# Kernel tuning notes

Hardware: AMD Instinct MI355X
Metric: run time of the kernel (lower is better)

The kernel has to match this reference:

```python
import jax, jax.numpy as jnp
import numpy as np

IN_DIM = 64
OUT_DIM = 64
N_MODES = 32


def setup_inputs() -> dict:
    key = jax.random.key(0)
    k_x, k_w0, k_w1 = jax.random.split(key, 3)
    x = jax.random.normal(k_x, (32, IN_DIM, 128, 128), dtype=jnp.float32)
    # xavier_normal_ on tensor of shape (in, out, modes, 2): fan_in = out*modes*2, fan_out = in*modes*2? 
    # torch treats dim0 as fan_out-ish; exact init scale is irrelevant for correctness baselines,
    # so use a matching gaussian std = sqrt(2/(in_dim+out_dim)).
    std = float(np.sqrt(2.0 / (IN_DIM + OUT_DIM)))
    w0 = std * jax.random.normal(k_w0, (IN_DIM, OUT_DIM, N_MODES, 2), dtype=jnp.float32)
    w1 = std * jax.random.normal(k_w1, (IN_DIM, OUT_DIM, N_MODES, 2), dtype=jnp.float32)
    return {"x": x, "w0": w0, "w1": w1}


def reference(x, w0, w1):
    B, I, M, N = x.shape
    n_modes = w0.shape[2]

    # ---- width (last-axis) branch ----
    x_fty = jnp.fft.rfft(x, axis=-1, norm='ortho')                      # [B, I, M, N//2+1]
    wc0 = w0[..., 0] + 1j * w0[..., 1]                                  # [I, O, n_modes]
    low_y = jnp.einsum('bixy,ioy->boxy', x_fty[..., :n_modes], wc0)     # [B, O, M, n_modes]
    out_ft_y = jnp.pad(low_y, ((0, 0), (0, 0), (0, 0), (0, N // 2 + 1 - n_modes)))
    xy = jnp.fft.irfft(out_ft_y, n=N, axis=-1, norm='ortho')            # [B, O, M, N]

    # ---- height (second-to-last axis) branch ----
    x_ftx = jnp.fft.rfft(x, axis=-2, norm='ortho')                      # [B, I, M//2+1, N]
    wc1 = w1[..., 0] + 1j * w1[..., 1]                                  # [I, O, n_modes]
    low_x = jnp.einsum('bixy,iox->boxy', x_ftx[:, :, :n_modes, :], wc1)  # [B, O, n_modes, N]
    out_ft_x = jnp.pad(low_x, ((0, 0), (0, 0), (0, M // 2 + 1 - n_modes), (0, 0)))
    xx = jnp.fft.irfft(out_ft_x, n=M, axis=-2, norm='ortho')            # [B, O, M, N]

    return xx + xy
```

## Files before the change

kernel.cpp:

```cpp
#include <hip/hip_runtime.h>


typedef _Float16 half8  __attribute__((ext_vector_type(8)));
typedef _Float16 half4v __attribute__((ext_vector_type(4)));
typedef _Float16 half2v __attribute__((ext_vector_type(2)));
typedef float    floatx4 __attribute__((ext_vector_type(4)));

#define TWO_PI_OVER_128 0.049087385212340517f

__device__ __forceinline__ unsigned int packh2(float a, float b) {
    half2v h; h[0] = (_Float16)a; h[1] = (_Float16)b;
    return __builtin_bit_cast(unsigned int, h);
}
__device__ __forceinline__ half8  ash8(uint4 u) { return __builtin_bit_cast(half8, u); }
__device__ __forceinline__ half4v ash4(uint2 u) { return __builtin_bit_cast(half4v, u); }

#define MFMA_K16(A,B,C) __builtin_amdgcn_mfma_f32_16x16x16f16((A),(B),(C),0,0,0)

#define YS_PK 324
#define YS_PR 20

__global__ __launch_bounds__(256) void w2expand(const float* __restrict__ w0,
                                                const float* __restrict__ w1,
                                                uint2* __restrict__ W2h)
{
    int g = blockIdx.x * 256 + threadIdx.x;
    const float* w = (g >> 17) ? w1 : w0;
    int e    = g & 131071;
    int lane = e & 63;
    int m    = (e >> 6) & 7;
    int c    = (e >> 9) & 7;
    int k    = e >> 12;
    int mrow = lane & 15, q = lane >> 4;
    int o  = (m * 16 + mrow) >> 1;
    int oc = mrow & 1;
    unsigned int h2[2];
#pragma unroll
    for (int hp = 0; hp < 2; ++hp) {
        int i = c * 8 + q * 2 + hp;
        const float* wp = w + ((i * 64 + o) * 32 + k) * 2;
        float re = wp[0], im = wp[1];
        float v0 = oc ? im : re;
        float v1 = oc ? re : -im;
        h2[hp] = packh2(v0, v1);
    }
    W2h[g] = make_uint2(h2[0], h2[1]);
}

template<int BR>
__global__ __launch_bounds__(1024, 4) void spectral(const float* __restrict__ x,
                                                    const uint2* __restrict__ w2,
                                                    float* __restrict__ out)
{
    __shared__ uint4 Ubuf[36864 / 16];
    __shared__ unsigned short Ys[32 * YS_PK];

    unsigned short* Xs = (unsigned short*)Ubuf;
    unsigned int*   Zs = (unsigned int*)Ubuf;

    const int tid  = threadIdx.x;
    const int wv   = tid >> 6;
    const int lane = tid & 63;
    const int mrow = tid & 15;
    const int quad = (tid >> 4) & 3;
    const int bx   = blockIdx.x;
    const int b    = bx >> 3;
    const int tile = bx & 7;

    const long xb = (long)b * 1048576 + (BR == 0 ? tile * 2048 : tile * 16);
    const long ob = xb;

    const int kptile = wv & 3;
    half8 Ff[4];
#pragma unroll
    for (int s = 0; s < 4; ++s)
#pragma unroll
        for (int j = 0; j < 8; ++j) {
            int d  = s * 32 + quad * 8 + j;
            int kp = kptile * 16 + mrow;
            int k  = kp >> 1;
            float ang = TWO_PI_OVER_128 * (float)((k * d) & 127);
            float v = (kp & 1) ? -sinf(ang) : cosf(ang);
            Ff[s][j] = (_Float16)v;
        }

    floatx4 acc[2][8];
#pragma unroll
    for (int kk = 0; kk < 2; ++kk)
#pragma unroll
        for (int m = 0; m < 8; ++m)
            acc[kk][m] = (floatx4){0.f, 0.f, 0.f, 0.f};

    if (BR == 0) {
#pragma unroll
        for (int p = 0; p < 4; ++p) {
            int idx = p * 1024 + tid;
            int col = idx >> 5, dg = idx & 31;
            int i = col >> 4, t = col & 15;
            const float4 v = *(const float4*)(x + xb + (long)i * 16384 + t * 128 + dg * 4);
            *(uint2*)&Xs[col * 136 + dg * 4] = make_uint2(packh2(v.x, v.y), packh2(v.z, v.w));
        }
    } else {
#pragma unroll
        for (int p = 0; p < 4; ++p) {
            int i  = (tid >> 9) + p * 2;
            int d  = (tid >> 2) & 127;
            int tq = (tid & 3) * 4;
            const float4 v = *(const float4*)(x + xb + (long)i * 16384 + d * 128 + tq);
            int colb = i * 16 + tq;
            Xs[(colb + 0) * 136 + d] = __builtin_bit_cast(unsigned short, (_Float16)v.x);
            Xs[(colb + 1) * 136 + d] = __builtin_bit_cast(unsigned short, (_Float16)v.y);
            Xs[(colb + 2) * 136 + d] = __builtin_bit_cast(unsigned short, (_Float16)v.z);
            Xs[(colb + 3) * 136 + d] = __builtin_bit_cast(unsigned short, (_Float16)v.w);
        }
    }
    __syncthreads();

    for (int c = 0; c < 8; ++c) {
#pragma unroll
        for (int cc = 0; cc < 2; ++cc) {
            int i = (wv >> 2) * 2 + cc;
            floatx4 y4 = {0.f, 0.f, 0.f, 0.f};
#pragma unroll
            for (int s = 0; s < 4; ++s) {
                uint4 bv = *(const uint4*)&Xs[(i * 16 + mrow) * 136 + s * 32 + quad * 8];
                y4 = __builtin_amdgcn_mfma_f32_16x16x32_f16(Ff[s], ash8(bv), y4, 0, 0, 0);
            }
            int k0 = kptile * 8 + quad * 2;
            unsigned int* yw = (unsigned int*)Ys;
            yw[(k0    ) * (YS_PK / 2) + mrow * (YS_PR / 2) + i] = packh2(y4[0], y4[1]);
            yw[(k0 + 1) * (YS_PK / 2) + mrow * (YS_PR / 2) + i] = packh2(y4[2], y4[3]);
        }
        __syncthreads();

        float4 pf[4];
        if (c < 7) {
            if (BR == 0) {
#pragma unroll
                for (int p = 0; p < 4; ++p) {
                    int idx = p * 1024 + tid;
                    int col = idx >> 5, dg = idx & 31;
                    int i = col >> 4, t = col & 15;
                    pf[p] = *(const float4*)(x + xb + (long)((c + 1) * 8 + i) * 16384 + t * 128 + dg * 4);
                }
            } else {
#pragma unroll
                for (int p = 0; p < 4; ++p) {
                    int i  = (tid >> 9) + p * 2;
                    int d  = (tid >> 2) & 127;
                    int tq = (tid & 3) * 4;
                    pf[p] = *(const float4*)(x + xb + (long)((c + 1) * 8 + i) * 16384 + d * 128 + tq);
                }
            }
        }

        {
            half4v bf0 = ash4(*(const uint2*)&Ys[(wv * 2    ) * YS_PK + mrow * YS_PR + quad * 4]);
            half4v bf1 = ash4(*(const uint2*)&Ys[(wv * 2 + 1) * YS_PK + mrow * YS_PR + quad * 4]);
            const uint2* wp = w2 + (((2 * wv) * 8 + c) * 8) * 64 + lane;
#pragma unroll
            for (int m = 0; m < 8; ++m) {
                uint2 a0u = wp[m * 64];
                uint2 a1u = wp[m * 64 + 4096];
                acc[0][m] = MFMA_K16(ash4(a0u), bf0, acc[0][m]);
                acc[1][m] = MFMA_K16(ash4(a1u), bf1, acc[1][m]);
            }
        }

        if (c < 7) {
            if (BR == 0) {
#pragma unroll
                for (int p = 0; p < 4; ++p) {
                    int idx = p * 1024 + tid;
                    int col = idx >> 5, dg = idx & 31;
                    *(uint2*)&Xs[col * 136 + dg * 4] =
                        make_uint2(packh2(pf[p].x, pf[p].y), packh2(pf[p].z, pf[p].w));
                }
            } else {
#pragma unroll
                for (int p = 0; p < 4; ++p) {
                    int d  = (tid >> 2) & 127;
                    int tq = (tid & 3) * 4;
                    int colb = ((tid >> 9) + p * 2) * 16 + tq;
                    Xs[(colb + 0) * 136 + d] = __builtin_bit_cast(unsigned short, (_Float16)pf[p].x);
                    Xs[(colb + 1) * 136 + d] = __builtin_bit_cast(unsigned short, (_Float16)pf[p].y);
                    Xs[(colb + 2) * 136 + d] = __builtin_bit_cast(unsigned short, (_Float16)pf[p].z);
                    Xs[(colb + 3) * 136 + d] = __builtin_bit_cast(unsigned short, (_Float16)pf[p].w);
                }
            }
        }
        __syncthreads();
    }

    const int dt  = wv & 7;
    const int ctb = (wv >> 3) * 8;
    const int dp  = dt * 16 + mrow;
    half8 Gf[2];
#pragma unroll
    for (int s = 0; s < 2; ++s)
#pragma unroll
        for (int j = 0; j < 8; ++j) {
            int kp = s * 32 + quad * 8 + j;
            int k  = kp >> 1;
            float ang = TWO_PI_OVER_128 * (float)((k * dp) & 127);
            float v;
            if (kp == 0)      v = 1.f / 128.f;
            else if (kp == 1) v = 0.f;
            else v = (kp & 1) ? -(2.f / 128.f) * sinf(ang) : (2.f / 128.f) * cosf(ang);
            Gf[s][j] = (_Float16)v;
        }

    for (int q = 0; q < 4; ++q) {
        __syncthreads();
#pragma unroll
        for (int mm = 0; mm < 2; ++mm) {
            const int m = q * 2 + mm;
#pragma unroll
            for (int kk = 0; kk < 2; ++kk) {
                const int slot = (wv * 2 + kk) ^ (quad * 8);
                const int col  = (mm * 8 + quad * 2) * 16 + mrow;
                Zs[ col       * 36 + slot] = packh2(acc[kk][m][0], acc[kk][m][1]);
                Zs[(col + 16) * 36 + slot] = packh2(acc[kk][m][2], acc[kk][m][3]);
            }
        }
        __syncthreads();

#pragma unroll
        for (int cc = 0; cc < 8; ++cc) {
            const int ct  = ctb + cc;
            const int col = ct * 16 + mrow;
            const int swz = (ct & 6) << 2;
            floatx4 o4 = {0.f, 0.f, 0.f, 0.f};
#pragma unroll
            for (int s = 0; s < 2; ++s) {
                uint4 zv = *(const uint4*)&Zs[col * 36 + ((s * 16 + quad * 4) ^ swz)];
                o4 = __builtin_amdgcn_mfma_f32_16x16x32_f16(Gf[s], ash8(zv), o4, 0, 0, 0);
            }
            const int oo = q * 16 + ct;
            const int t  = mrow;
            const int db = dt * 16 + quad * 4;
            if (BR == 0) {
                __builtin_nontemporal_store(o4, (floatx4*)(out + ob + (long)oo * 16384 + t * 128 + db));
            } else {
                float* p = out + ob + (long)oo * 16384 + (long)db * 128 + t;
                unsafeAtomicAdd(p,       o4[0]);
                unsafeAtomicAdd(p + 128, o4[1]);
                unsafeAtomicAdd(p + 256, o4[2]);
                unsafeAtomicAdd(p + 384, o4[3]);
            }
        }
    }
}

extern "C" void kernel_launch(void* const* d_in, const int* in_sizes, int n_in,
                              void* d_out, int out_size, void* d_ws, size_t ws_size,
                              hipStream_t stream) {
    const float* x  = (const float*)d_in[0];
    const float* w0 = (const float*)d_in[1];
    const float* w1 = (const float*)d_in[2];
    float* out = (float*)d_out;

    uint2* W2h = (uint2*)d_ws;

    w2expand<<<dim3(1024), dim3(256), 0, stream>>>(w0, w1, W2h);

    dim3 grid(256);
    dim3 block(1024);

    spectral<0><<<grid, block, 0, stream>>>(x, W2h,          out);
    spectral<1><<<grid, block, 0, stream>>>(x, W2h + 131072, out);
}
```

Before: 577.9 us.

## Split output channels across two 512-thread blocks per tile

Each spatial tile is now handled by two 512-thread blocks, each covering half of the output channels, which doubles the grid to 512 blocks. Each block redoes the forward DFT for all input channels, with every wave covering four input-channel slices instead of two, and computes only its half of the channel mixing and inverse transform. The prefetch of the next input chunk is split into two halves placed around the DFT and mixing phases. The goal is better occupancy and load balance across CUs, paid for by duplicating the forward-transform work and the input reads for every tile.

```diff
diff --git a/kernel.cpp b/kernel.cpp
--- a/kernel.cpp
+++ b/kernel.cpp
@@ -48,11 +48,11 @@
 }
 
 template<int BR>
-__global__ __launch_bounds__(1024, 4) void spectral(const float* __restrict__ x,
-                                                    const uint2* __restrict__ w2,
-                                                    float* __restrict__ out)
+__global__ __launch_bounds__(512, 4) void spectral(const float* __restrict__ x,
+                                                   const uint2* __restrict__ w2,
+                                                   float* __restrict__ out)
 {
-    __shared__ uint4 Ubuf[36864 / 16];
+    __shared__ uint4 Ubuf[34816 / 16];
     __shared__ unsigned short Ys[32 * YS_PK];
 
     unsigned short* Xs = (unsigned short*)Ubuf;
@@ -64,8 +64,9 @@
     const int mrow = tid & 15;
     const int quad = (tid >> 4) & 3;
     const int bx   = blockIdx.x;
-    const int b    = bx >> 3;
-    const int tile = bx & 7;
+    const int oh   = bx & 1;
+    const int tile = (bx >> 1) & 7;
+    const int b    = bx >> 4;
 
     const long xb = (long)b * 1048576 + (BR == 0 ? tile * 2048 : tile * 16);
     const long ob = xb;
@@ -84,42 +85,70 @@
             Ff[s][j] = (_Float16)v;
         }
 
-    floatx4 acc[2][8];
-#pragma unroll
-    for (int kk = 0; kk < 2; ++kk)
-#pragma unroll
-        for (int m = 0; m < 8; ++m)
-            acc[kk][m] = (floatx4){0.f, 0.f, 0.f, 0.f};
-
-    if (BR == 0) {
-#pragma unroll
-        for (int p = 0; p < 4; ++p) {
-            int idx = p * 1024 + tid;
-            int col = idx >> 5, dg = idx & 31;
-            int i = col >> 4, t = col & 15;
-            const float4 v = *(const float4*)(x + xb + (long)i * 16384 + t * 128 + dg * 4);
-            *(uint2*)&Xs[col * 136 + dg * 4] = make_uint2(packh2(v.x, v.y), packh2(v.z, v.w));
-        }
-    } else {
-#pragma unroll
-        for (int p = 0; p < 4; ++p) {
-            int i  = (tid >> 9) + p * 2;
-            int d  = (tid >> 2) & 127;
-            int tq = (tid & 3) * 4;
-            const float4 v = *(const float4*)(x + xb + (long)i * 16384 + d * 128 + tq);
-            int colb = i * 16 + tq;
-            Xs[(colb + 0) * 136 + d] = __builtin_bit_cast(unsigned short, (_Float16)v.x);
-            Xs[(colb + 1) * 136 + d] = __builtin_bit_cast(unsigned short, (_Float16)v.y);
-            Xs[(colb + 2) * 136 + d] = __builtin_bit_cast(unsigned short, (_Float16)v.z);
-            Xs[(colb + 3) * 136 + d] = __builtin_bit_cast(unsigned short, (_Float16)v.w);
+    floatx4 acc[2][2][4];
+#pragma unroll
+    for (int a = 0; a < 2; ++a)
+#pragma unroll
+        for (int kk = 0; kk < 2; ++kk)
+#pragma unroll
+            for (int m = 0; m < 4; ++m)
+                acc[a][kk][m] = (floatx4){0.f, 0.f, 0.f, 0.f};
+
+
+#pragma unroll
+    for (int g = 0; g < 2; ++g) {
+        float4 v[4];
+#pragma unroll
+        for (int pp = 0; pp < 4; ++pp) {
+            int p = g * 4 + pp;
+            if (BR == 0) {
+                int idx = p * 512 + tid;
+                int col = idx >> 5, dg = idx & 31;
+                v[pp] = *(const float4*)(x + xb + (long)(col >> 4) * 16384 + (col & 15) * 128 + dg * 4);
+            } else {
+                int d = (tid >> 2) & 127, tq = (tid & 3) * 4;
+                v[pp] = *(const float4*)(x + xb + (long)p * 16384 + d * 128 + tq);
+            }
+        }
+#pragma unroll
+        for (int pp = 0; pp < 4; ++pp) {
+            int p = g * 4 + pp;
+            if (BR == 0) {
+                int idx = p * 512 + tid;
+                int col = idx >> 5, dg = idx & 31;
+                *(uint2*)&Xs[col * 136 + dg * 4] =
+                    make_uint2(packh2(v[pp].x, v[pp].y), packh2(v[pp].z, v[pp].w));
+            } else {
+                int d = (tid >> 2) & 127, tq = (tid & 3) * 4;
+                int colb = p * 16 + tq;
+                Xs[(colb + 0) * 136 + d] = __builtin_bit_cast(unsigned short, (_Float16)v[pp].x);
+                Xs[(colb + 1) * 136 + d] = __builtin_bit_cast(unsigned short, (_Float16)v[pp].y);
+                Xs[(colb + 2) * 136 + d] = __builtin_bit_cast(unsigned short, (_Float16)v[pp].z);
+                Xs[(colb + 3) * 136 + d] = __builtin_bit_cast(unsigned short, (_Float16)v[pp].w);
+            }
         }
     }
     __syncthreads();
 
     for (int c = 0; c < 8; ++c) {
-#pragma unroll
-        for (int cc = 0; cc < 2; ++cc) {
-            int i = (wv >> 2) * 2 + cc;
+        float4 pfA[4];
+        if (c < 7) {
+#pragma unroll
+            for (int p = 0; p < 4; ++p) {
+                if (BR == 0) {
+                    int idx = p * 512 + tid;
+                    int col = idx >> 5, dg = idx & 31;
+                    pfA[p] = *(const float4*)(x + xb + (long)((c + 1) * 8 + (col >> 4)) * 16384 + (col & 15) * 128 + dg * 4);
+                } else {
+                    int d = (tid >> 2) & 127, tq = (tid & 3) * 4;
+                    pfA[p] = *(const float4*)(x + xb + (long)((c + 1) * 8 + p) * 16384 + d * 128 + tq);
+                }
+            }
+        }
+
+#pragma unroll
+        for (int cc = 0; cc < 4; ++cc) {
+            int i = (wv >> 2) * 4 + cc;
             floatx4 y4 = {0.f, 0.f, 0.f, 0.f};
 #pragma unroll
             for (int s = 0; s < 4; ++s) {
@@ -133,68 +162,76 @@
         }
         __syncthreads();
 
-        float4 pf[4];
+        float4 pfB[4];
         if (c < 7) {
-            if (BR == 0) {
-#pragma unroll
-                for (int p = 0; p < 4; ++p) {
-                    int idx = p * 1024 + tid;
-                    int col = idx >> 5, dg = idx & 31;
-                    int i = col >> 4, t = col & 15;
-                    pf[p] = *(const float4*)(x + xb + (long)((c + 1) * 8 + i) * 16384 + t * 128 + dg * 4);
-                }
-            } else {
-#pragma unroll
-                for (int p = 0; p < 4; ++p) {
-                    int i  = (tid >> 9) + p * 2;
-                    int d  = (tid >> 2) & 127;
-                    int tq = (tid & 3) * 4;
-                    pf[p] = *(const float4*)(x + xb + (long)((c + 1) * 8 + i) * 16384 + d * 128 + tq);
-                }
-            }
-        }
-
-        {
-            half4v bf0 = ash4(*(const uint2*)&Ys[(wv * 2    ) * YS_PK + mrow * YS_PR + quad * 4]);
-            half4v bf1 = ash4(*(const uint2*)&Ys[(wv * 2 + 1) * YS_PK + mrow * YS_PR + quad * 4]);
-            const uint2* wp = w2 + (((2 * wv) * 8 + c) * 8) * 64 + lane;
-#pragma unroll
-            for (int m = 0; m < 8; ++m) {
-                uint2 a0u = wp[m * 64];
-                uint2 a1u = wp[m * 64 + 4096];
-                acc[0][m] = MFMA_K16(ash4(a0u), bf0, acc[0][m]);
-                acc[1][m] = MFMA_K16(ash4(a1u), bf1, acc[1][m]);
-            }
-        }
-
-        if (c < 7) {
-            if (BR == 0) {
-#pragma unroll
-                for (int p = 0; p < 4; ++p) {
-                    int idx = p * 1024 + tid;
+#pragma unroll
+            for (int p = 0; p < 4; ++p) {
+                if (BR == 0) {
+                    int idx = p * 512 + tid;
                     int col = idx >> 5, dg = idx & 31;
                     *(uint2*)&Xs[col * 136 + dg * 4] =
-                        make_uint2(packh2(pf[p].x, pf[p].y), packh2(pf[p].z, pf[p].w));
+                        make_uint2(packh2(pfA[p].x, pfA[p].y), packh2(pfA[p].z, pfA[p].w));
+                } else {
+                    int d = (tid >> 2) & 127, tq = (tid & 3) * 4;
+                    int colb = p * 16 + tq;
+                    Xs[(colb + 0) * 136 + d] = __builtin_bit_cast(unsigned short, (_Float16)pfA[p].x);
+                    Xs[(colb + 1) * 136 + d] = __builtin_bit_cast(unsigned short, (_Float16)pfA[p].y);
+                    Xs[(colb + 2) * 136 + d] = __builtin_bit_cast(unsigned short, (_Float16)pfA[p].z);
+                    Xs[(colb + 3) * 136 + d] = __builtin_bit_cast(unsigned short, (_Float16)pfA[p].w);
                 }
-            } else {
-#pragma unroll
-                for (int p = 0; p < 4; ++p) {
-                    int d  = (tid >> 2) & 127;
-                    int tq = (tid & 3) * 4;
-                    int colb = ((tid >> 9) + p * 2) * 16 + tq;
-                    Xs[(colb + 0) * 136 + d] = __builtin_bit_cast(unsigned short, (_Float16)pf[p].x);
-                    Xs[(colb + 1) * 136 + d] = __builtin_bit_cast(unsigned short, (_Float16)pf[p].y);
-                    Xs[(colb + 2) * 136 + d] = __builtin_bit_cast(unsigned short, (_Float16)pf[p].z);
-                    Xs[(colb + 3) * 136 + d] = __builtin_bit_cast(unsigned short, (_Float16)pf[p].w);
+            }
+#pragma unroll
+            for (int p = 0; p < 4; ++p) {
+                if (BR == 0) {
+                    int idx = (p + 4) * 512 + tid;
+                    int col = idx >> 5, dg = idx & 31;
+                    pfB[p] = *(const float4*)(x + xb + (long)((c + 1) * 8 + (col >> 4)) * 16384 + (col & 15) * 128 + dg * 4);
+                } else {
+                    int d = (tid >> 2) & 127, tq = (tid & 3) * 4;
+                    pfB[p] = *(const float4*)(x + xb + (long)((c + 1) * 8 + 4 + p) * 16384 + d * 128 + tq);
+                }
+            }
+        }
+
+        {
+            half4v bfA0 = ash4(*(const uint2*)&Ys[(2 * wv     ) * YS_PK + mrow * YS_PR + quad * 4]);
+            half4v bfA1 = ash4(*(const uint2*)&Ys[(2 * wv + 1 ) * YS_PK + mrow * YS_PR + quad * 4]);
+            half4v bfB0 = ash4(*(const uint2*)&Ys[(2 * wv + 16) * YS_PK + mrow * YS_PR + quad * 4]);
+            half4v bfB1 = ash4(*(const uint2*)&Ys[(2 * wv + 17) * YS_PK + mrow * YS_PR + quad * 4]);
+            const uint2* wpA = w2 + (((2 * wv) * 8 + c) * 8 + oh * 4) * 64 + lane;
+            const uint2* wpB = wpA + 65536;
+#pragma unroll
+            for (int m = 0; m < 4; ++m) {
+                acc[0][0][m] = MFMA_K16(ash4(wpA[m * 64       ]), bfA0, acc[0][0][m]);
+                acc[0][1][m] = MFMA_K16(ash4(wpA[m * 64 + 4096]), bfA1, acc[0][1][m]);
+                acc[1][0][m] = MFMA_K16(ash4(wpB[m * 64       ]), bfB0, acc[1][0][m]);
+                acc[1][1][m] = MFMA_K16(ash4(wpB[m * 64 + 4096]), bfB1, acc[1][1][m]);
+            }
+        }
+
+        if (c < 7) {
+#pragma unroll
+            for (int p = 0; p < 4; ++p) {
+                if (BR == 0) {
+                    int idx = (p + 4) * 512 + tid;
+                    int col = idx >> 5, dg = idx & 31;
+                    *(uint2*)&Xs[col * 136 + dg * 4] =
+                        make_uint2(packh2(pfB[p].x, pfB[p].y), packh2(pfB[p].z, pfB[p].w));
+                } else {
+                    int d = (tid >> 2) & 127, tq = (tid & 3) * 4;
+                    int colb = (4 + p) * 16 + tq;
+                    Xs[(colb + 0) * 136 + d] = __builtin_bit_cast(unsigned short, (_Float16)pfB[p].x);
+                    Xs[(colb + 1) * 136 + d] = __builtin_bit_cast(unsigned short, (_Float16)pfB[p].y);
+                    Xs[(colb + 2) * 136 + d] = __builtin_bit_cast(unsigned short, (_Float16)pfB[p].z);
+                    Xs[(colb + 3) * 136 + d] = __builtin_bit_cast(unsigned short, (_Float16)pfB[p].w);
                 }
             }
         }
         __syncthreads();
     }
 
-    const int dt  = wv & 7;
-    const int ctb = (wv >> 3) * 8;
-    const int dp  = dt * 16 + mrow;
+    const int dt = wv;
+    const int dp = dt * 16 + mrow;
     half8 Gf[2];
 #pragma unroll
     for (int s = 0; s < 2; ++s)
@@ -210,24 +247,24 @@
             Gf[s][j] = (_Float16)v;
         }
 
+#pragma unroll
     for (int q = 0; q < 4; ++q) {
         __syncthreads();
 #pragma unroll
-        for (int mm = 0; mm < 2; ++mm) {
-            const int m = q * 2 + mm;
+        for (int a = 0; a < 2; ++a)
 #pragma unroll
             for (int kk = 0; kk < 2; ++kk) {
-                const int slot = (wv * 2 + kk) ^ (quad * 8);
-                const int col  = (mm * 8 + quad * 2) * 16 + mrow;
-                Zs[ col       * 36 + slot] = packh2(acc[kk][m][0], acc[kk][m][1]);
-                Zs[(col + 16) * 36 + slot] = packh2(acc[kk][m][2], acc[kk][m][3]);
-            }
-        }
+                const int kmode = 2 * (wv + a * 8) + kk;
+                const int slot  = kmode ^ (quad * 8);
+                const int col   = (quad * 2) * 16 + mrow;
+                Zs[ col       * 36 + slot] = packh2(acc[a][kk][q][0], acc[a][kk][q][1]);
+                Zs[(col + 16) * 36 + slot] = packh2(acc[a][kk][q][2], acc[a][kk][q][3]);
+            }
         __syncthreads();
 
 #pragma unroll
         for (int cc = 0; cc < 8; ++cc) {
-            const int ct  = ctb + cc;
+            const int ct  = cc;
             const int col = ct * 16 + mrow;
             const int swz = (ct & 6) << 2;
             floatx4 o4 = {0.f, 0.f, 0.f, 0.f};
@@ -236,7 +273,7 @@
                 uint4 zv = *(const uint4*)&Zs[col * 36 + ((s * 16 + quad * 4) ^ swz)];
                 o4 = __builtin_amdgcn_mfma_f32_16x16x32_f16(Gf[s], ash8(zv), o4, 0, 0, 0);
             }
-            const int oo = q * 16 + ct;
+            const int oo = oh * 32 + q * 8 + ct;
             const int t  = mrow;
             const int db = dt * 16 + quad * 4;
             if (BR == 0) {
@@ -264,8 +301,8 @@
 
     w2expand<<<dim3(1024), dim3(256), 0, stream>>>(w0, w1, W2h);
 
-    dim3 grid(256);
-    dim3 block(1024);
+    dim3 grid(512);
+    dim3 block(512);
 
     spectral<0><<<grid, block, 0, stream>>>(x, W2h,          out);
     spectral<1><<<grid, block, 0, stream>>>(x, W2h + 131072, out);
```

Result: no change. 574.5 us (-0.6%).
